# Optimization experiments

Measured on AMD Instinct MI355X. Metric: run time of the kernel, lower is better.

Reference implementation:

```python
import jax, jax.numpy as jnp
import numpy as np

EMBEDDING = 1024
PARAMETERS = 4096

def setup_inputs() -> dict:
    key = jax.random.key(0)
    kx, kK, kV = jax.random.split(key, 3)
    x = jax.random.normal(kx, (4, 2048, EMBEDDING), dtype=jnp.float32)
    K = jax.random.normal(kK, (PARAMETERS, EMBEDDING), dtype=jnp.float32)
    V = jax.random.normal(kV, (PARAMETERS, EMBEDDING), dtype=jnp.float32)
    return {"x": x, "K": K, "V": V}

def reference(x, K, V):
    # scores: [b, s, p] = scale * x @ K.T
    scale = EMBEDDING ** (-0.5)
    scores = scale * jnp.einsum('bse,pe->bsp', x, K)
    attn = jax.nn.softmax(scores, axis=-1)
    # out: [b, s, e] = attn @ V
    return jnp.einsum('bsp,pe->bse', attn, V)
```

## Files before the change

kernel.cpp:

```cpp
#include <hip/hip_runtime.h>
#include <hip/hip_bf16.h>

typedef __bf16 bf16x8 __attribute__((ext_vector_type(8)));
typedef __bf16 bf16x4 __attribute__((ext_vector_type(4)));
typedef float floatx4 __attribute__((ext_vector_type(4)));

__device__ __forceinline__ void async16(void* lds, const void* g) {
  __builtin_amdgcn_global_load_lds(
      (const __attribute__((address_space(1))) unsigned int*)g,
      (__attribute__((address_space(3))) unsigned int*)lds, 16, 0, 0);
}

__global__ __launch_bounds__(256) void preprocess_kernel(
    const float* __restrict__ x, const float* __restrict__ Kp,
    const float* __restrict__ V, __bf16* __restrict__ xb,
    __bf16* __restrict__ Kb, __bf16* __restrict__ Vt,
    float* __restrict__ lsum, float* __restrict__ outz) {
  const int b = blockIdx.x;
  const int t = threadIdx.x;
  if (b < 2048) {
#pragma unroll
    for (int k = 0; k < 4; ++k) {
      const int i = b * 1024 + k * 256 + t;
      float4 v = ((const float4*)x)[i];
      bf16x4 o = {(__bf16)v.x, (__bf16)v.y, (__bf16)v.z, (__bf16)v.w};
      ((bf16x4*)xb)[i] = o;
    }
  } else if (b < 3072) {
#pragma unroll
    for (int k = 0; k < 4; ++k) {
      const int i = (b - 2048) * 1024 + k * 256 + t;
      float4 v = ((const float4*)Kp)[i];
      bf16x4 o = {(__bf16)v.x, (__bf16)v.y, (__bf16)v.z, (__bf16)v.w};
      ((bf16x4*)Kb)[i] = o;
    }
  } else if (b < 4096) {
    __shared__ float tile[64][65];
    const int bb = b - 3072;
    const int bx = bb & 63, by = bb >> 6;
    for (int i = t; i < 64 * 64; i += 256) {
      const int r = i >> 6, c = i & 63;
      tile[r][c] = V[(size_t)(bx * 64 + r) * 1024 + by * 64 + c];
    }
    __syncthreads();
    for (int i = t; i < 64 * 64; i += 256) {
      const int r = i >> 6, c = i & 63;
      Vt[(size_t)(by * 64 + r) * 4096 + bx * 64 + c] = (__bf16)tile[c][r];
    }
  } else if (b == 4096) {
#pragma unroll
    for (int k = 0; k < 8; ++k)
      ((floatx4*)lsum)[k * 256 + t] = floatx4{0.f, 0.f, 0.f, 0.f};
  } else {
    const size_t bb = b - 4097;
#pragma unroll
    for (int k = 0; k < 4; ++k)
      ((float4*)outz)[bb * 1024 + k * 256 + t] = float4{0.f, 0.f, 0.f, 0.f};
  }
}

template <int MODE, int LD, int KR, int NS, int MTX, int SPL>
__global__ __launch_bounds__(512, 2) void gemm_kernel(const __bf16* __restrict__ A,
                                                      const __bf16* __restrict__ B,
                                                      __bf16* __restrict__ Cb,
                                                      float* __restrict__ Cf,
                                                      float* __restrict__ lsum) {
  constexpr int NT = KR / 64;
  __shared__ char lds[131072];

  const int t = threadIdx.x;
  const int lane = t & 63;
  const int w = t >> 6;
  const int wm = w >> 2;
  const int wn = w & 3;

  const int id = blockIdx.x;
  const int g = id & 7;
  const int s = id >> 3;
  const int ks = s % SPL;
  const int r2 = s / SPL;
  const int mt = g * MTX + (r2 % MTX);
  const int nt = r2 / MTX;
  const int m0 = mt * 256;
  const int n0 = nt * 256;
  const size_t koff = (size_t)ks * KR;

  const int v = (t & 7) ^ ((t >> 3) & 7);
  const int srow = 2 * (t >> 3) + (v >> 2);
  const int sk8 = (v & 3) * 8;
  const __bf16* aS = A + (size_t)(m0 + srow) * LD + koff + sk8;
  const __bf16* bS = B + (size_t)(n0 + srow) * LD + koff + sk8;
  const int t16 = t * 16;

  auto stageA = [&](int slot, int kElem) {
    const __bf16* p = aS + kElem;
    async16(lds + slot + t16, p);
    async16(lds + slot + 8192 + t16, p + (size_t)128 * LD);
  };
  auto stageB = [&](int slot, int kElem) {
    const __bf16* p = bS + kElem;
    async16(lds + slot + t16, p);
    async16(lds + slot + 8192 + t16, p + (size_t)128 * LD);
  };

  const int rl = lane & 15;
  const int qq = lane >> 4;
  const int fo = (rl >> 1) * 128 + (((((rl & 1) << 2) | qq) ^ (rl >> 1)) << 4);
  const int aOff = wm * 8192 + fo;
  const int bOff = wn * 4096 + fo;

  floatx4 acc[8][4] = {};

  stageA(0, 0);          stageB(32768, 0);
  stageA(16384, 32);     stageB(49152, 32);
  stageA(65536, 64);     stageB(98304, 64);
  asm volatile("s_waitcnt vmcnt(8)" ::: "memory");
  __builtin_amdgcn_s_barrier();

  for (int T = 0; T < NT; ++T) {
    const int bas = (T & 1) << 16;
    const int oth = bas ^ 65536;
    const int kT = T * 64;
    bf16x8 aF[4], bF[4];

#pragma unroll
    for (int i = 0; i < 4; ++i) aF[i] = *(const bf16x8*)(lds + bas + aOff + i * 1024);
#pragma unroll
    for (int j = 0; j < 4; ++j) bF[j] = *(const bf16x8*)(lds + bas + 32768 + bOff + j * 1024);
    if (T + 1 < NT) stageA(oth + 16384, kT + 96);
    __builtin_amdgcn_s_barrier();
    asm volatile("s_waitcnt lgkmcnt(0)" ::: "memory");
    __builtin_amdgcn_sched_barrier(0);
    __builtin_amdgcn_s_setprio(1);
#pragma unroll
    for (int i = 0; i < 4; ++i)
#pragma unroll
      for (int j = 0; j < 4; ++j)
        acc[i][j] = __builtin_amdgcn_mfma_f32_16x16x32_bf16(aF[i], bF[j], acc[i][j], 0, 0, 0);
    __builtin_amdgcn_s_setprio(0);
    __builtin_amdgcn_s_barrier();

#pragma unroll
    for (int i = 0; i < 4; ++i) aF[i] = *(const bf16x8*)(lds + bas + aOff + 4096 + i * 1024);
    if (T + 1 < NT) stageB(oth + 49152, kT + 96);
    if (T == NT - 1) asm volatile("s_waitcnt vmcnt(0)" ::: "memory");
    else             asm volatile("s_waitcnt vmcnt(8)" ::: "memory");
    __builtin_amdgcn_s_barrier();
    asm volatile("s_waitcnt lgkmcnt(0)" ::: "memory");
    __builtin_amdgcn_sched_barrier(0);
    __builtin_amdgcn_s_setprio(1);
#pragma unroll
    for (int i = 0; i < 4; ++i)
#pragma unroll
      for (int j = 0; j < 4; ++j)
        acc[4 + i][j] = __builtin_amdgcn_mfma_f32_16x16x32_bf16(aF[i], bF[j], acc[4 + i][j], 0, 0, 0);
    __builtin_amdgcn_s_setprio(0);
    __builtin_amdgcn_s_barrier();

#pragma unroll
    for (int i = 0; i < 4; ++i) aF[i] = *(const bf16x8*)(lds + bas + 16384 + aOff + i * 1024);
#pragma unroll
    for (int j = 0; j < 4; ++j) bF[j] = *(const bf16x8*)(lds + bas + 49152 + bOff + j * 1024);
    if (T + 2 < NT) stageA(bas, kT + 128);
    __builtin_amdgcn_s_barrier();
    asm volatile("s_waitcnt lgkmcnt(0)" ::: "memory");
    __builtin_amdgcn_sched_barrier(0);
    __builtin_amdgcn_s_setprio(1);
#pragma unroll
    for (int i = 0; i < 4; ++i)
#pragma unroll
      for (int j = 0; j < 4; ++j)
        acc[i][j] = __builtin_amdgcn_mfma_f32_16x16x32_bf16(aF[i], bF[j], acc[i][j], 0, 0, 0);
    __builtin_amdgcn_s_setprio(0);
    __builtin_amdgcn_s_barrier();

#pragma unroll
    for (int i = 0; i < 4; ++i) aF[i] = *(const bf16x8*)(lds + bas + 16384 + aOff + 4096 + i * 1024);
    if (T + 2 < NT) stageB(bas + 32768, kT + 128);
    if (T + 2 < NT)      asm volatile("s_waitcnt vmcnt(8)" ::: "memory");
    else if (T + 1 < NT) asm volatile("s_waitcnt vmcnt(4)" ::: "memory");
    __builtin_amdgcn_s_barrier();
    asm volatile("s_waitcnt lgkmcnt(0)" ::: "memory");
    __builtin_amdgcn_sched_barrier(0);
    __builtin_amdgcn_s_setprio(1);
#pragma unroll
    for (int i = 0; i < 4; ++i)
#pragma unroll
      for (int j = 0; j < 4; ++j)
        acc[4 + i][j] = __builtin_amdgcn_mfma_f32_16x16x32_bf16(aF[i], bF[j], acc[4 + i][j], 0, 0, 0);
    __builtin_amdgcn_s_setprio(0);
    __builtin_amdgcn_s_barrier();
  }

  const int cmB = wm * 128 + ((lane >> 4) << 2);
  const int cn = n0 + wn * 64 + (lane & 15);
  if (MODE == 0) {
#pragma unroll
    for (int i = 0; i < 8; ++i)
#pragma unroll
      for (int r = 0; r < 4; ++r) {
        const int m = m0 + cmB + i * 16 + r;
        float rs = 0.f;
#pragma unroll
        for (int j = 0; j < 4; ++j) {
          const float e = __expf(fminf(acc[i][j][r] * 0.03125f, 30.0f));
          rs += e;
          Cb[(size_t)m * NS + cn + j * 16] = (__bf16)e;
        }
        rs += __shfl_xor(rs, 1, 64);
        rs += __shfl_xor(rs, 2, 64);
        rs += __shfl_xor(rs, 4, 64);
        rs += __shfl_xor(rs, 8, 64);
        if ((lane & 15) == 0) atomicAdd(&lsum[m], rs);
      }
  } else {
#pragma unroll
    for (int i = 0; i < 8; ++i)
#pragma unroll
      for (int r = 0; r < 4; ++r) {
        const int m = m0 + cmB + i * 16 + r;
        const float inv = 1.0f / lsum[m];
#pragma unroll
        for (int j = 0; j < 4; ++j)
          atomicAdd(&Cf[(size_t)m * NS + cn + j * 16], acc[i][j][r] * inv);
      }
  }
}

extern "C" void kernel_launch(void* const* d_in, const int* in_sizes, int n_in,
                              void* d_out, int out_size, void* d_ws, size_t ws_size,
                              hipStream_t stream) {
  const float* x = (const float*)d_in[0];
  const float* K = (const float*)d_in[1];
  const float* V = (const float*)d_in[2];
  float* out = (float*)d_out;

  char* ws = (char*)d_ws;
  __bf16* xb = (__bf16*)ws;
  __bf16* Kb = (__bf16*)(ws + (16u << 20));
  __bf16* Vt = (__bf16*)(ws + (24u << 20));
  __bf16* P  = (__bf16*)(ws + (32u << 20));
  float*  l  = (float*)(ws + (96u << 20));

  preprocess_kernel<<<6145, 256, 0, stream>>>(x, K, V, xb, Kb, Vt, l, out);
  gemm_kernel<0, 1024, 1024, 4096, 4, 1><<<512, 512, 0, stream>>>(xb, Kb, P, nullptr, l);
  gemm_kernel<1, 4096, 2048, 1024, 4, 2><<<256, 512, 0, stream>>>(P, Vt, nullptr, out, l);
}
```

Measured before the change: 290.0 us.

## Double-buffer LDS fragment registers to overlap reads with MFMA

Result: no change. 287.2 us (-0.9%).

```diff
diff --git a/kernel.cpp b/kernel.cpp
--- a/kernel.cpp
+++ b/kernel.cpp
@@ -117,77 +117,72 @@
   asm volatile("s_waitcnt vmcnt(8)" ::: "memory");
   __builtin_amdgcn_s_barrier();
 
+  bf16x8 aA[4], aB[4], bX[4], bY[4];
+#pragma unroll
+  for (int i = 0; i < 4; ++i) aA[i] = *(const bf16x8*)(lds + aOff + i * 1024);
+#pragma unroll
+  for (int j = 0; j < 4; ++j) bX[j] = *(const bf16x8*)(lds + 32768 + bOff + j * 1024);
+
   for (int T = 0; T < NT; ++T) {
     const int bas = (T & 1) << 16;
     const int oth = bas ^ 65536;
     const int kT = T * 64;
-    bf16x8 aF[4], bF[4];
-
-#pragma unroll
-    for (int i = 0; i < 4; ++i) aF[i] = *(const bf16x8*)(lds + bas + aOff + i * 1024);
-#pragma unroll
-    for (int j = 0; j < 4; ++j) bF[j] = *(const bf16x8*)(lds + bas + 32768 + bOff + j * 1024);
+
+#pragma unroll
+    for (int i = 0; i < 4; ++i) aB[i] = *(const bf16x8*)(lds + bas + aOff + 4096 + i * 1024);
     if (T + 1 < NT) stageA(oth + 16384, kT + 96);
-    __builtin_amdgcn_s_barrier();
-    asm volatile("s_waitcnt lgkmcnt(0)" ::: "memory");
-    __builtin_amdgcn_sched_barrier(0);
-    __builtin_amdgcn_s_setprio(1);
-#pragma unroll
-    for (int i = 0; i < 4; ++i)
-#pragma unroll
-      for (int j = 0; j < 4; ++j)
-        acc[i][j] = __builtin_amdgcn_mfma_f32_16x16x32_bf16(aF[i], bF[j], acc[i][j], 0, 0, 0);
-    __builtin_amdgcn_s_setprio(0);
-    __builtin_amdgcn_s_barrier();
-
-#pragma unroll
-    for (int i = 0; i < 4; ++i) aF[i] = *(const bf16x8*)(lds + bas + aOff + 4096 + i * 1024);
+    __builtin_amdgcn_s_setprio(1);
+#pragma unroll
+    for (int i = 0; i < 4; ++i)
+#pragma unroll
+      for (int j = 0; j < 4; ++j)
+        acc[i][j] = __builtin_amdgcn_mfma_f32_16x16x32_bf16(aA[i], bX[j], acc[i][j], 0, 0, 0);
+    __builtin_amdgcn_s_setprio(0);
+    if (T + 1 < NT) asm volatile("s_waitcnt vmcnt(6)" ::: "memory");
+    else            asm volatile("s_waitcnt vmcnt(0)" ::: "memory");
+    __builtin_amdgcn_s_barrier();
+
+#pragma unroll
+    for (int i = 0; i < 4; ++i) aA[i] = *(const bf16x8*)(lds + bas + 16384 + aOff + i * 1024);
+#pragma unroll
+    for (int j = 0; j < 4; ++j) bY[j] = *(const bf16x8*)(lds + bas + 49152 + bOff + j * 1024);
     if (T + 1 < NT) stageB(oth + 49152, kT + 96);
-    if (T == NT - 1) asm volatile("s_waitcnt vmcnt(0)" ::: "memory");
-    else             asm volatile("s_waitcnt vmcnt(8)" ::: "memory");
-    __builtin_amdgcn_s_barrier();
-    asm volatile("s_waitcnt lgkmcnt(0)" ::: "memory");
-    __builtin_amdgcn_sched_barrier(0);
-    __builtin_amdgcn_s_setprio(1);
-#pragma unroll
-    for (int i = 0; i < 4; ++i)
-#pragma unroll
-      for (int j = 0; j < 4; ++j)
-        acc[4 + i][j] = __builtin_amdgcn_mfma_f32_16x16x32_bf16(aF[i], bF[j], acc[4 + i][j], 0, 0, 0);
-    __builtin_amdgcn_s_setprio(0);
-    __builtin_amdgcn_s_barrier();
-
-#pragma unroll
-    for (int i = 0; i < 4; ++i) aF[i] = *(const bf16x8*)(lds + bas + 16384 + aOff + i * 1024);
-#pragma unroll
-    for (int j = 0; j < 4; ++j) bF[j] = *(const bf16x8*)(lds + bas + 49152 + bOff + j * 1024);
+    __builtin_amdgcn_s_setprio(1);
+#pragma unroll
+    for (int i = 0; i < 4; ++i)
+#pragma unroll
+      for (int j = 0; j < 4; ++j)
+        acc[4 + i][j] = __builtin_amdgcn_mfma_f32_16x16x32_bf16(aB[i], bX[j], acc[4 + i][j], 0, 0, 0);
+    __builtin_amdgcn_s_setprio(0);
+    __builtin_amdgcn_s_barrier();
+
+#pragma unroll
+    for (int i = 0; i < 4; ++i) aB[i] = *(const bf16x8*)(lds + bas + 16384 + aOff + 4096 + i * 1024);
     if (T + 2 < NT) stageA(bas, kT + 128);
-    __builtin_amdgcn_s_barrier();
-    asm volatile("s_waitcnt lgkmcnt(0)" ::: "memory");
-    __builtin_amdgcn_sched_barrier(0);
-    __builtin_amdgcn_s_setprio(1);
-#pragma unroll
-    for (int i = 0; i < 4; ++i)
-#pragma unroll
-      for (int j = 0; j < 4; ++j)
-        acc[i][j] = __builtin_amdgcn_mfma_f32_16x16x32_bf16(aF[i], bF[j], acc[i][j], 0, 0, 0);
-    __builtin_amdgcn_s_setprio(0);
-    __builtin_amdgcn_s_barrier();
-
-#pragma unroll
-    for (int i = 0; i < 4; ++i) aF[i] = *(const bf16x8*)(lds + bas + 16384 + aOff + 4096 + i * 1024);
+    __builtin_amdgcn_s_setprio(1);
+#pragma unroll
+    for (int i = 0; i < 4; ++i)
+#pragma unroll
+      for (int j = 0; j < 4; ++j)
+        acc[i][j] = __builtin_amdgcn_mfma_f32_16x16x32_bf16(aA[i], bY[j], acc[i][j], 0, 0, 0);
+    __builtin_amdgcn_s_setprio(0);
+    if (T + 2 < NT)      asm volatile("s_waitcnt vmcnt(6)" ::: "memory");
+    else if (T + 1 < NT) asm volatile("s_waitcnt vmcnt(4)" ::: "memory");
+    __builtin_amdgcn_s_barrier();
+
+    if (T + 1 < NT) {
+#pragma unroll
+      for (int i = 0; i < 4; ++i) aA[i] = *(const bf16x8*)(lds + oth + aOff + i * 1024);
+#pragma unroll
+      for (int j = 0; j < 4; ++j) bX[j] = *(const bf16x8*)(lds + oth + 32768 + bOff + j * 1024);
+    }
     if (T + 2 < NT) stageB(bas + 32768, kT + 128);
-    if (T + 2 < NT)      asm volatile("s_waitcnt vmcnt(8)" ::: "memory");
-    else if (T + 1 < NT) asm volatile("s_waitcnt vmcnt(4)" ::: "memory");
-    __builtin_amdgcn_s_barrier();
-    asm volatile("s_waitcnt lgkmcnt(0)" ::: "memory");
-    __builtin_amdgcn_sched_barrier(0);
-    __builtin_amdgcn_s_setprio(1);
-#pragma unroll
-    for (int i = 0; i < 4; ++i)
-#pragma unroll
-      for (int j = 0; j < 4; ++j)
-        acc[4 + i][j] = __builtin_amdgcn_mfma_f32_16x16x32_bf16(aF[i], bF[j], acc[4 + i][j], 0, 0, 0);
+    __builtin_amdgcn_s_setprio(1);
+#pragma unroll
+    for (int i = 0; i < 4; ++i)
+#pragma unroll
+      for (int j = 0; j < 4; ++j)
+        acc[4 + i][j] = __builtin_amdgcn_mfma_f32_16x16x32_bf16(aB[i], bY[j], acc[4 + i][j], 0, 0, 0);
     __builtin_amdgcn_s_setprio(0);
     __builtin_amdgcn_s_barrier();
   }
```
